# Kernel optimization log

Hardware: AMD Instinct MI355X
Metric: run time of the kernel (lower is better)

Reference implementation:

```python
import jax, jax.numpy as jnp
import numpy as np

MASK_VAL = -1e18


def _soft_nn(src, src_mask, tgt, tgt_mask):
    """score[b,i,j] = -mean_d (src[b,i,d]-tgt[b,j,d])^2, masked softmax over j,
    then soft nearest neighbor = weights @ tgt.  Uses the |a|^2+|b|^2-2ab
    expansion instead of materializing the [B,M,N,D] broadcast tensor."""
    D = src.shape[-1]
    sq_s = jnp.sum(src * src, axis=-1)                 # [B,M]
    sq_t = jnp.sum(tgt * tgt, axis=-1)                 # [B,N]
    dots = jnp.einsum('bid,bjd->bij', src, tgt)        # [B,M,N]
    dist = (sq_s[:, :, None] + sq_t[:, None, :] - 2.0 * dots) / D
    valid = (src_mask[:, :, None] > 0) & (tgt_mask[:, None, :] > 0)
    score = jnp.where(valid, -dist, MASK_VAL)
    weights = jax.nn.softmax(score, axis=-1)           # [B,M,N]
    nn = jnp.einsum('bij,bjd->bid', weights, tgt)      # [B,M,D]
    return nn, weights


def _cycle_loss(mask, lens, beta):
    """Expected index under beta vs. original index; only the diagonal of the
    original [B,M,M] distance matrix survives, so compute it directly."""
    M = mask.shape[-1]
    idx = jnp.arange(M, dtype=beta.dtype)              # [M]
    index_nn = jnp.einsum('j,bij->bi', idx, beta)      # [B,M]
    l_seq = jnp.square(index_nn - idx[None, :]) * (mask > 0)  # diag of masked dist
    return jnp.mean(jnp.sum(l_seq, axis=-1) / lens)


def setup_inputs() -> dict:
    key = jax.random.key(0)
    kce, kse, kcl, ksl = jax.random.split(key, 4)
    B, M, N, D = 32, 1024, 1024, 128
    clip_lens = jax.random.randint(kcl, (B,), M // 2, M + 1)
    sent_lens = jax.random.randint(ksl, (B,), N // 2, N + 1)
    # original code requires max(lens) == padded length (idx_orig broadcast)
    clip_lens = clip_lens.at[0].set(M)
    sent_lens = sent_lens.at[0].set(N)
    clip_mask = (jnp.arange(M)[None, :] < clip_lens[:, None]).astype(jnp.float32)
    sent_mask = (jnp.arange(N)[None, :] < sent_lens[:, None]).astype(jnp.float32)
    return {
        'clip_emb': jax.random.normal(kce, (B, M, D), dtype=jnp.float32),
        'clip_mask': clip_mask,
        'clip_lens': clip_lens.astype(jnp.float32),
        'sent_emb': jax.random.normal(kse, (B, N, D), dtype=jnp.float32),
        'sent_mask': sent_mask,
        'sent_lens': sent_lens.astype(jnp.float32),
    }


def reference(clip_emb, clip_mask, clip_lens, sent_emb, sent_mask, sent_lens):
    # clip -> sent -> clip cycle
    clip_sent_nn, _ = _soft_nn(clip_emb, clip_mask, sent_emb, sent_mask)
    _, clip_beta = _soft_nn(clip_sent_nn, clip_mask, clip_emb, clip_mask)
    clip_clip_loss = _cycle_loss(clip_mask, clip_lens, clip_beta)
    # sent -> clip -> sent cycle
    sent_clip_nn, _ = _soft_nn(sent_emb, sent_mask, clip_emb, clip_mask)
    _, sent_beta = _soft_nn(sent_clip_nn, sent_mask, sent_emb, sent_mask)
    sent_sent_loss = _cycle_loss(sent_mask, sent_lens, sent_beta)
    return (clip_clip_loss, sent_sent_loss)
```

## Files before the change

### kernel.cpp

```cpp
#include <hip/hip_runtime.h>
#include <hip/hip_bf16.h>
#include <math.h>

typedef __attribute__((ext_vector_type(16))) float f32x16;
typedef __attribute__((ext_vector_type(8))) short short8;
typedef __attribute__((ext_vector_type(4))) short short4v;
typedef __attribute__((ext_vector_type(4))) unsigned uint4v;

#define BATCH 32
#define SEQ 1024
#define DIM 128
#define NBLK 512
#define TILE_BYTES 16384
#define CDOT 0.02254211097f
#define SQE_SCALE 0.011271055485f

__device__ __forceinline__ float exp2f_fast(float x) {
  float r;
  asm("v_exp_f32 %0, %1" : "=v"(r) : "v"(x));
  return r;
}

__device__ __forceinline__ unsigned cvt_pk_bf16(float lo, float hi) {
  unsigned r;
  asm("v_cvt_pk_bf16_f32 %0, %1, %2" : "=v"(r) : "v"(lo), "v"(hi));
  return r;
}

__device__ __forceinline__ unsigned vs_off(int j, int k) {
  return ((unsigned)(k >> 4) << 11) + ((unsigned)j << 5)
       + ((((unsigned)(k & 15)) << 1) ^ ((((unsigned)j >> 2) & 1) << 4));
}

__device__ __forceinline__ short4v ds_tr16(unsigned addr) {
  short4v r;
  asm volatile("ds_read_b64_tr_b16 %0, %1" : "=v"(r) : "v"(addr));
  return r;
}

typedef __attribute__((address_space(1))) const unsigned int gu32;
typedef __attribute__((address_space(3))) unsigned int lu32;
__device__ __forceinline__ void gload_lds16(const void* g, void* l) {
  __builtin_amdgcn_global_load_lds((gu32*)g, (lu32*)l, 16, 0, 0);
}

__global__ __launch_bounds__(256)
void prepack_kernel(const float* __restrict__ clip, const float* __restrict__ sent,
                    char* __restrict__ outN, float* __restrict__ sqe_all) {
  const int bid = blockIdx.x;
  const int tid = threadIdx.x;
  const float* inp = (bid < NBLK) ? clip : sent;
  const size_t row0 = (size_t)(bid & (NBLK - 1)) * 64;
  char* ot = outN + (size_t)bid * TILE_BYTES;
  #pragma unroll
  for (int it = 0; it < 8; ++it) {
    int idx = it * 256 + tid;
    int j = idx >> 5, q = idx & 31;
    float4 v = *reinterpret_cast<const float4*>(inp + (row0 + j) * DIM + q * 4);
    uint2 pk;
    pk.x = cvt_pk_bf16(v.x, v.y);
    pk.y = cvt_pk_bf16(v.z, v.w);
    *reinterpret_cast<uint2*>(ot + vs_off(j, q * 4)) = pk;
    float s = v.x * v.x + v.y * v.y + v.z * v.z + v.w * v.w;
    #pragma unroll
    for (int off = 1; off < 32; off <<= 1) s += __shfl_xor(s, off);
    if ((tid & 31) == 0) sqe_all[bid * 64 + j] = s * SQE_SCALE;
  }
}

__global__ __launch_bounds__(256, 2)
void cycle_kernel(const char* __restrict__ embN, const float* __restrict__ sqe_all,
                  const float* __restrict__ clip_lens, const float* __restrict__ sent_lens,
                  float* __restrict__ partials)
{
  __shared__ __align__(16) char VS[2][TILE_BYTES];
  __shared__ __align__(16) float SQL[2][SEQ];
  __shared__ __align__(16) char MG[32768];
  __shared__ float RED[4][4][64];

  const int tid = threadIdx.x;
  const int x = blockIdx.x;
  const int rest = x >> 3;
  const int b    = (x & 7) + 8 * ((rest >> 2) & 3);
  const int cyc  = (rest >> 4) & 1;
  const int qh   = (rest & 3) | (((rest >> 5) & 1) << 2);

  const char* srcN = embN + (cyc ? (size_t)NBLK * TILE_BYTES : 0);
  const char* othN = embN + (cyc ? 0 : (size_t)NBLK * TILE_BYTES);
  const float* sqe_src = sqe_all + (cyc ? BATCH * SEQ : 0) + b * SEQ;
  const float* sqe_oth = sqe_all + (cyc ? 0 : BATCH * SEQ) + b * SEQ;
  const float* lens_src = cyc ? sent_lens : clip_lens;
  const float* lens_oth = cyc ? clip_lens : sent_lens;

  const int w = tid >> 6, l = tid & 63;
  const int p = w >> 1, h = w & 1;
  const int il = l & 31, hi = l >> 5, g1 = (l >> 4) & 1;

  const char* src_tiles = srcN + (size_t)(b * 16) * TILE_BYTES;
  const char* oth_tiles = othN + (size_t)(b * 16) * TILE_BYTES;

  const int nv1 = (int)(lens_oth[b] + 0.5f);
  const int nv2 = (int)(lens_src[b] + 0.5f);
  const int nt1 = (nv1 + 63) >> 6;
  const int nt2 = (nv2 + 63) >> 6;

  auto STAGE = [&](int buf, const char* gt) {
    #pragma unroll
    for (int i = 0; i < 4; ++i)
      gload_lds16(gt + i * 4096 + tid * 16, &VS[buf][i * 4096 + tid * 16]);
  };

  STAGE(0, oth_tiles);
  {
    float4 vo = reinterpret_cast<const float4*>(sqe_oth)[tid];
    float4 vq = reinterpret_cast<const float4*>(sqe_src)[tid];
    reinterpret_cast<float4*>(&SQL[0][0])[tid] = vo;
    reinterpret_cast<float4*>(&SQL[1][0])[tid] = vq;
  }

  const unsigned qk0 = (unsigned)(il * 32 + ((hi * 16) ^ (((il >> 2) & 1) << 4)));
  const int t16 = (l & 8) ? -16 : 16;

  short8 aq[2][8];
  {
    const char* qt = src_tiles + (size_t)(qh * 2 + p) * TILE_BYTES;
    #pragma unroll
    for (int s = 0; s < 2; ++s) {
      const unsigned qoff = (unsigned)((s * 32 + il) * 32
                            + ((hi * 16) ^ (((il >> 2) & 1) << 4)));
      #pragma unroll
      for (int kc = 0; kc < 8; ++kc)
        aq[s][kc] = *reinterpret_cast<const short8*>(qt + qoff + kc * 2048);
    }
  }

  f32x16 nn[2][4];
  #pragma unroll
  for (int s = 0; s < 2; ++s)
    #pragma unroll
    for (int d = 0; d < 4; ++d)
      #pragma unroll
      for (int r = 0; r < 16; ++r) nn[s][d][r] = 0.f;
  float lsum[2] = {0.f, 0.f};

  asm volatile("s_waitcnt vmcnt(0)" ::: "memory");
  __syncthreads();

  int cur = 0;
  for (int t = 0; t < nt1; ++t) {
    const int jb = t * 64;
    if (t + 1 < nt1) STAGE(cur ^ 1, oth_tiles + (size_t)(t + 1) * TILE_BYTES);
    else             STAGE(cur ^ 1, src_tiles);

    const char* vsc = &VS[cur][0];
    const unsigned vsb = (unsigned)(size_t)vsc;
    const unsigned trb0 = vsb + (unsigned)(g1 * 1920);
    const unsigned trb1 = trb0 + (unsigned)(128 + t16);
    const bool partial = (jb + h * 32 + 32) > nv1;

    f32x16 sa0, sa1;
    #pragma unroll
    for (int r = 0; r < 16; ++r) { sa0[r] = 0.f; sa1[r] = 0.f; }
    __builtin_amdgcn_s_setprio(1);
    #pragma unroll
    for (int kc = 0; kc < 8; ++kc) {
      short8 ka = *reinterpret_cast<const short8*>(vsc + qk0 + h * 1024 + kc * 2048);
      sa0 = __builtin_amdgcn_mfma_f32_32x32x16_bf16(ka, aq[0][kc], sa0, 0, 0, 0);
      sa1 = __builtin_amdgcn_mfma_f32_32x32x16_bf16(ka, aq[1][kc], sa1, 0, 0, 0);
    }
    __builtin_amdgcn_s_setprio(0);
    #pragma unroll
    for (int q = 0; q < 4; ++q) {
      float4 sq4 = *reinterpret_cast<const float4*>(&SQL[0][jb + h * 32 + q * 8 + hi * 4]);
      sa0[q*4+0] = exp2f_fast(fmaf(sa0[q*4+0], CDOT, -sq4.x));
      sa0[q*4+1] = exp2f_fast(fmaf(sa0[q*4+1], CDOT, -sq4.y));
      sa0[q*4+2] = exp2f_fast(fmaf(sa0[q*4+2], CDOT, -sq4.z));
      sa0[q*4+3] = exp2f_fast(fmaf(sa0[q*4+3], CDOT, -sq4.w));
      sa1[q*4+0] = exp2f_fast(fmaf(sa1[q*4+0], CDOT, -sq4.x));
      sa1[q*4+1] = exp2f_fast(fmaf(sa1[q*4+1], CDOT, -sq4.y));
      sa1[q*4+2] = exp2f_fast(fmaf(sa1[q*4+2], CDOT, -sq4.z));
      sa1[q*4+3] = exp2f_fast(fmaf(sa1[q*4+3], CDOT, -sq4.w));
    }
    if (partial) {
      #pragma unroll
      for (int r = 0; r < 16; ++r) {
        int j = jb + h * 32 + (r & 3) + 8 * (r >> 2) + 4 * hi;
        if (j >= nv1) { sa0[r] = 0.f; sa1[r] = 0.f; }
      }
    }
    float ls0 = 0.f, ls1 = 0.f;
    #pragma unroll
    for (int r = 0; r < 16; ++r) { ls0 += sa0[r]; ls1 += sa1[r]; }
    lsum[0] += ls0; lsum[1] += ls1;

    #pragma unroll
    for (int gm = 0; gm < 2; ++gm) {
      const int kap = h * 2 + gm;
      short4v t0[4], t1[4];
      #pragma unroll
      for (int dblk = 0; dblk < 4; ++dblk) {
        t0[dblk] = ds_tr16(trb0 + (unsigned)(dblk * 4096 + kap * 512));
        t1[dblk] = ds_tr16(trb1 + (unsigned)(dblk * 4096 + kap * 512));
      }
      unsigned a00 = cvt_pk_bf16(sa0[gm*8+0], sa0[gm*8+1]);
      unsigned a01 = cvt_pk_bf16(sa0[gm*8+2], sa0[gm*8+3]);
      unsigned a10 = cvt_pk_bf16(sa0[gm*8+4], sa0[gm*8+5]);
      unsigned a11 = cvt_pk_bf16(sa0[gm*8+6], sa0[gm*8+7]);
      asm volatile("v_permlane32_swap_b32 %0, %1" : "+v"(a00), "+v"(a10));
      asm volatile("v_permlane32_swap_b32 %0, %1" : "+v"(a01), "+v"(a11));
      uint4v pw0; pw0.x = a00; pw0.y = a01; pw0.z = a10; pw0.w = a11;
      short8 paf0 = __builtin_bit_cast(short8, pw0);
      unsigned b00 = cvt_pk_bf16(sa1[gm*8+0], sa1[gm*8+1]);
      unsigned b01 = cvt_pk_bf16(sa1[gm*8+2], sa1[gm*8+3]);
      unsigned b10 = cvt_pk_bf16(sa1[gm*8+4], sa1[gm*8+5]);
      unsigned b11 = cvt_pk_bf16(sa1[gm*8+6], sa1[gm*8+7]);
      asm volatile("v_permlane32_swap_b32 %0, %1" : "+v"(b00), "+v"(b10));
      asm volatile("v_permlane32_swap_b32 %0, %1" : "+v"(b01), "+v"(b11));
      uint4v pw1; pw1.x = b00; pw1.y = b01; pw1.z = b10; pw1.w = b11;
      short8 paf1 = __builtin_bit_cast(short8, pw1);

      asm volatile("s_waitcnt lgkmcnt(0)" ::: "memory");
      __builtin_amdgcn_sched_barrier(0);
      __builtin_amdgcn_s_setprio(1);
      #pragma unroll
      for (int dblk = 0; dblk < 4; ++dblk) {
        short8 vf = __builtin_shufflevector(t0[dblk], t1[dblk], 0, 1, 2, 3, 4, 5, 6, 7);
        nn[0][dblk] = __builtin_amdgcn_mfma_f32_32x32x16_bf16(vf, paf0, nn[0][dblk], 0, 0, 0);
        nn[1][dblk] = __builtin_amdgcn_mfma_f32_32x32x16_bf16(vf, paf1, nn[1][dblk], 0, 0, 0);
      }
      __builtin_amdgcn_s_setprio(0);
    }

    asm volatile("s_waitcnt vmcnt(0)" ::: "memory");
    __syncthreads();
    cur ^= 1;
  }

  RED[w][0][l] = lsum[0];
  RED[w][1][l] = lsum[1];
  #pragma unroll
  for (int c = 0; c < 4; ++c) {
    const int s = c >> 1, d0 = (c & 1) * 2;
    #pragma unroll
    for (int hf = 0; hf < 2; ++hf) {
      const f32x16 v = nn[s][d0 + hf];
      #pragma unroll
      for (int i = 0; i < 4; ++i) {
        float4 f4;
        f4.x = v[i*4+0]; f4.y = v[i*4+1]; f4.z = v[i*4+2]; f4.w = v[i*4+3];
        *reinterpret_cast<float4*>(MG + w * 8192 + (hf * 4 + i) * 1024 + l * 16) = f4;
      }
    }
    __syncthreads();
    #pragma unroll
    for (int hf = 0; hf < 2; ++hf) {
      #pragma unroll
      for (int i = 0; i < 4; ++i) {
        float4 f4 = *reinterpret_cast<const float4*>(
            MG + (w ^ 1) * 8192 + (hf * 4 + i) * 1024 + l * 16);
        nn[s][d0+hf][i*4+0] += f4.x;
        nn[s][d0+hf][i*4+1] += f4.y;
        nn[s][d0+hf][i*4+2] += f4.z;
        nn[s][d0+hf][i*4+3] += f4.w;
      }
    }
    __syncthreads();
  }
  lsum[0] += RED[w ^ 1][0][l];
  lsum[1] += RED[w ^ 1][1][l];

  short8 aq2[2][8];
  #pragma unroll
  for (int s = 0; s < 2; ++s) {
    lsum[s] += __shfl_xor(lsum[s], 32);
    const float inv1 = 1.f / lsum[s];
    #pragma unroll
    for (int kc = 0; kc < 8; ++kc) {
      const int dblk = kc >> 1, gm = kc & 1;
      unsigned u00 = cvt_pk_bf16(nn[s][dblk][gm*8+0] * inv1, nn[s][dblk][gm*8+1] * inv1);
      unsigned u01 = cvt_pk_bf16(nn[s][dblk][gm*8+2] * inv1, nn[s][dblk][gm*8+3] * inv1);
      unsigned u10 = cvt_pk_bf16(nn[s][dblk][gm*8+4] * inv1, nn[s][dblk][gm*8+5] * inv1);
      unsigned u11 = cvt_pk_bf16(nn[s][dblk][gm*8+6] * inv1, nn[s][dblk][gm*8+7] * inv1);
      asm volatile("v_permlane32_swap_b32 %0, %1" : "+v"(u00), "+v"(u10));
      asm volatile("v_permlane32_swap_b32 %0, %1" : "+v"(u01), "+v"(u11));
      uint4v pw; pw.x = u00; pw.y = u01; pw.z = u10; pw.w = u11;
      aq2[s][kc] = __builtin_bit_cast(short8, pw);
    }
  }

  float l2s[2] = {0.f, 0.f}, ixs[2] = {0.f, 0.f};
  for (int t = 0; t < nt2; ++t) {
    const int jb = t * 64;
    if (t + 1 < nt2) STAGE(cur ^ 1, src_tiles + (size_t)(t + 1) * TILE_BYTES);

    const char* vsc = &VS[cur][0];
    const bool partial = (jb + h * 32 + 32) > nv2;

    f32x16 sa0, sa1;
    #pragma unroll
    for (int r = 0; r < 16; ++r) { sa0[r] = 0.f; sa1[r] = 0.f; }
    __builtin_amdgcn_s_setprio(1);
    #pragma unroll
    for (int kc = 0; kc < 8; ++kc) {
      short8 ka = *reinterpret_cast<const short8*>(vsc + qk0 + h * 1024 + kc * 2048);
      sa0 = __builtin_amdgcn_mfma_f32_32x32x16_bf16(ka, aq2[0][kc], sa0, 0, 0, 0);
      sa1 = __builtin_amdgcn_mfma_f32_32x32x16_bf16(ka, aq2[1][kc], sa1, 0, 0, 0);
    }
    __builtin_amdgcn_s_setprio(0);
    #pragma unroll
    for (int q = 0; q < 4; ++q) {
      float4 sq4 = *reinterpret_cast<const float4*>(&SQL[1][jb + h * 32 + q * 8 + hi * 4]);
      sa0[q*4+0] = exp2f_fast(fmaf(sa0[q*4+0], CDOT, -sq4.x));
      sa0[q*4+1] = exp2f_fast(fmaf(sa0[q*4+1], CDOT, -sq4.y));
      sa0[q*4+2] = exp2f_fast(fmaf(sa0[q*4+2], CDOT, -sq4.z));
      sa0[q*4+3] = exp2f_fast(fmaf(sa0[q*4+3], CDOT, -sq4.w));
      sa1[q*4+0] = exp2f_fast(fmaf(sa1[q*4+0], CDOT, -sq4.x));
      sa1[q*4+1] = exp2f_fast(fmaf(sa1[q*4+1], CDOT, -sq4.y));
      sa1[q*4+2] = exp2f_fast(fmaf(sa1[q*4+2], CDOT, -sq4.z));
      sa1[q*4+3] = exp2f_fast(fmaf(sa1[q*4+3], CDOT, -sq4.w));
    }
    if (partial) {
      #pragma unroll
      for (int r = 0; r < 16; ++r) {
        int j = jb + h * 32 + (r & 3) + 8 * (r >> 2) + 4 * hi;
        if (j >= nv2) { sa0[r] = 0.f; sa1[r] = 0.f; }
      }
    }
    #pragma unroll
    for (int r = 0; r < 16; ++r) {
      float jc = (float)(jb + h * 32 + (r & 3) + 8 * (r >> 2) + 4 * hi);
      l2s[0] += sa0[r];
      l2s[1] += sa1[r];
      ixs[0] = fmaf(sa0[r], jc, ixs[0]);
      ixs[1] = fmaf(sa1[r], jc, ixs[1]);
    }

    asm volatile("s_waitcnt vmcnt(0)" ::: "memory");
    __syncthreads();
    cur ^= 1;
  }

  RED[w][0][l] = l2s[0]; RED[w][1][l] = l2s[1];
  RED[w][2][l] = ixs[0]; RED[w][3][l] = ixs[1];
  __syncthreads();
  l2s[0] += RED[w ^ 1][0][l]; l2s[1] += RED[w ^ 1][1][l];
  ixs[0] += RED[w ^ 1][2][l]; ixs[1] += RED[w ^ 1][3][l];

  float acc = 0.f;
  #pragma unroll
  for (int s = 0; s < 2; ++s) {
    l2s[s] += __shfl_xor(l2s[s], 32);
    ixs[s] += __shfl_xor(ixs[s], 32);
    int iabs = qh * 128 + p * 64 + s * 32 + il;
    float diff = ixs[s] / l2s[s] - (float)iabs;
    acc += (iabs < nv2) ? diff * diff : 0.f;
  }
  #pragma unroll
  for (int off = 1; off < 32; off <<= 1) acc += __shfl_xor(acc, off);
  if (h == 0 && l == 0)
    partials[cyc * 512 + (b * 8 + qh) * 2 + p] = acc / ((float)nv2 * (float)BATCH);
}

__global__ void reduce_kernel(const float* __restrict__ partials, float* __restrict__ out) {
  __shared__ float red[256];
  const int c = blockIdx.x;
  float s = 0.f;
  for (int i = threadIdx.x; i < 512; i += 256) s += partials[c * 512 + i];
  red[threadIdx.x] = s;
  __syncthreads();
  for (int off = 128; off > 0; off >>= 1) {
    if (threadIdx.x < off) red[threadIdx.x] += red[threadIdx.x + off];
    __syncthreads();
  }
  if (threadIdx.x == 0) out[c] = red[0];
}

extern "C" void kernel_launch(void* const* d_in, const int* in_sizes, int n_in,
                              void* d_out, int out_size, void* d_ws, size_t ws_size,
                              hipStream_t stream) {
  const float* clip_emb  = (const float*)d_in[0];
  const float* clip_lens = (const float*)d_in[2];
  const float* sent_emb  = (const float*)d_in[3];
  const float* sent_lens = (const float*)d_in[5];
  float* out = (float*)d_out;
  char* wsb = (char*)d_ws;

  char*  embN    = wsb;
  float* sqe_all = (float*)(wsb + 2 * (size_t)NBLK * TILE_BYTES);
  float* parts   = sqe_all + 2 * BATCH * SEQ;

  prepack_kernel<<<2 * NBLK, 256, 0, stream>>>(clip_emb, sent_emb, embN, sqe_all);
  cycle_kernel<<<NBLK, 256, 0, stream>>>(embN, sqe_all, clip_lens, sent_lens, parts);
  reduce_kernel<<<2, 256, 0, stream>>>(parts, out);
}
```

Measured before the change: 77.67 us.

## Stage 128-row tiles per barrier and reuse staging LDS for merge

Each pipeline stage now loads two 64-row tiles (32 KB) per buffer and processes them as two sub-tiles, halving the number of block-wide barriers and vmcnt waits in both cycle loops. The separate merge buffer is dropped; the cross-wave nn reduction reuses the idle staging buffer, so total LDS stays about the same. The s_setprio hints are removed and the transposed LDS reads are issued after the bf16 packing rather than before. In exchange, prefetch granularity is coarser, so more rows past the valid length may be loaded, and each stage has a longer unrolled body.

```diff
diff --git a/kernel.cpp b/kernel.cpp
--- a/kernel.cpp
+++ b/kernel.cpp
@@ -73,9 +73,8 @@
                   const float* __restrict__ clip_lens, const float* __restrict__ sent_lens,
                   float* __restrict__ partials)
 {
-  __shared__ __align__(16) char VS[2][TILE_BYTES];
+  __shared__ __align__(16) char VS[2][32768];
   __shared__ __align__(16) float SQL[2][SEQ];
-  __shared__ __align__(16) char MG[32768];
   __shared__ float RED[4][4][64];
 
   const int tid = threadIdx.x;
@@ -101,12 +100,12 @@
 
   const int nv1 = (int)(lens_oth[b] + 0.5f);
   const int nv2 = (int)(lens_src[b] + 0.5f);
-  const int nt1 = (nv1 + 63) >> 6;
-  const int nt2 = (nv2 + 63) >> 6;
+  const int nt1_2 = (nv1 + 127) >> 7;
+  const int nt2_2 = (nv2 + 127) >> 7;
 
   auto STAGE = [&](int buf, const char* gt) {
     #pragma unroll
-    for (int i = 0; i < 4; ++i)
+    for (int i = 0; i < 8; ++i)
       gload_lds16(gt + i * 4096 + tid * 16, &VS[buf][i * 4096 + tid * 16]);
   };
 
@@ -147,88 +146,89 @@
   __syncthreads();
 
   int cur = 0;
-  for (int t = 0; t < nt1; ++t) {
-    const int jb = t * 64;
-    if (t + 1 < nt1) STAGE(cur ^ 1, oth_tiles + (size_t)(t + 1) * TILE_BYTES);
-    else             STAGE(cur ^ 1, src_tiles);
-
-    const char* vsc = &VS[cur][0];
-    const unsigned vsb = (unsigned)(size_t)vsc;
-    const unsigned trb0 = vsb + (unsigned)(g1 * 1920);
-    const unsigned trb1 = trb0 + (unsigned)(128 + t16);
-    const bool partial = (jb + h * 32 + 32) > nv1;
-
-    f32x16 sa0, sa1;
-    #pragma unroll
-    for (int r = 0; r < 16; ++r) { sa0[r] = 0.f; sa1[r] = 0.f; }
-    __builtin_amdgcn_s_setprio(1);
-    #pragma unroll
-    for (int kc = 0; kc < 8; ++kc) {
-      short8 ka = *reinterpret_cast<const short8*>(vsc + qk0 + h * 1024 + kc * 2048);
-      sa0 = __builtin_amdgcn_mfma_f32_32x32x16_bf16(ka, aq[0][kc], sa0, 0, 0, 0);
-      sa1 = __builtin_amdgcn_mfma_f32_32x32x16_bf16(ka, aq[1][kc], sa1, 0, 0, 0);
-    }
-    __builtin_amdgcn_s_setprio(0);
-    #pragma unroll
-    for (int q = 0; q < 4; ++q) {
-      float4 sq4 = *reinterpret_cast<const float4*>(&SQL[0][jb + h * 32 + q * 8 + hi * 4]);
-      sa0[q*4+0] = exp2f_fast(fmaf(sa0[q*4+0], CDOT, -sq4.x));
-      sa0[q*4+1] = exp2f_fast(fmaf(sa0[q*4+1], CDOT, -sq4.y));
-      sa0[q*4+2] = exp2f_fast(fmaf(sa0[q*4+2], CDOT, -sq4.z));
-      sa0[q*4+3] = exp2f_fast(fmaf(sa0[q*4+3], CDOT, -sq4.w));
-      sa1[q*4+0] = exp2f_fast(fmaf(sa1[q*4+0], CDOT, -sq4.x));
-      sa1[q*4+1] = exp2f_fast(fmaf(sa1[q*4+1], CDOT, -sq4.y));
-      sa1[q*4+2] = exp2f_fast(fmaf(sa1[q*4+2], CDOT, -sq4.z));
-      sa1[q*4+3] = exp2f_fast(fmaf(sa1[q*4+3], CDOT, -sq4.w));
-    }
-    if (partial) {
-      #pragma unroll
-      for (int r = 0; r < 16; ++r) {
-        int j = jb + h * 32 + (r & 3) + 8 * (r >> 2) + 4 * hi;
-        if (j >= nv1) { sa0[r] = 0.f; sa1[r] = 0.f; }
+  for (int t = 0; t < nt1_2; ++t) {
+    if (t + 1 < nt1_2) STAGE(cur ^ 1, oth_tiles + (size_t)(t + 1) * 32768);
+    else               STAGE(cur ^ 1, src_tiles);
+
+    #pragma unroll
+    for (int sub = 0; sub < 2; ++sub) {
+      const int jb = t * 128 + sub * 64;
+      if (jb < nv1) {
+        const char* vsc = &VS[cur][0] + sub * 16384;
+        const unsigned vsb = (unsigned)(size_t)vsc;
+        const unsigned trb0 = vsb + (unsigned)(g1 * 1920);
+        const unsigned trb1 = trb0 + (unsigned)(128 + t16);
+        const bool partial = (jb + h * 32 + 32) > nv1;
+
+        f32x16 sa0, sa1;
+        #pragma unroll
+        for (int r = 0; r < 16; ++r) { sa0[r] = 0.f; sa1[r] = 0.f; }
+        #pragma unroll
+        for (int kc = 0; kc < 8; ++kc) {
+          short8 ka = *reinterpret_cast<const short8*>(vsc + qk0 + h * 1024 + kc * 2048);
+          sa0 = __builtin_amdgcn_mfma_f32_32x32x16_bf16(ka, aq[0][kc], sa0, 0, 0, 0);
+          sa1 = __builtin_amdgcn_mfma_f32_32x32x16_bf16(ka, aq[1][kc], sa1, 0, 0, 0);
+        }
+        #pragma unroll
+        for (int q = 0; q < 4; ++q) {
+          float4 sq4 = *reinterpret_cast<const float4*>(&SQL[0][jb + h * 32 + q * 8 + hi * 4]);
+          sa0[q*4+0] = exp2f_fast(fmaf(sa0[q*4+0], CDOT, -sq4.x));
+          sa0[q*4+1] = exp2f_fast(fmaf(sa0[q*4+1], CDOT, -sq4.y));
+          sa0[q*4+2] = exp2f_fast(fmaf(sa0[q*4+2], CDOT, -sq4.z));
+          sa0[q*4+3] = exp2f_fast(fmaf(sa0[q*4+3], CDOT, -sq4.w));
+          sa1[q*4+0] = exp2f_fast(fmaf(sa1[q*4+0], CDOT, -sq4.x));
+          sa1[q*4+1] = exp2f_fast(fmaf(sa1[q*4+1], CDOT, -sq4.y));
+          sa1[q*4+2] = exp2f_fast(fmaf(sa1[q*4+2], CDOT, -sq4.z));
+          sa1[q*4+3] = exp2f_fast(fmaf(sa1[q*4+3], CDOT, -sq4.w));
+        }
+        if (partial) {
+          #pragma unroll
+          for (int r = 0; r < 16; ++r) {
+            int j = jb + h * 32 + (r & 3) + 8 * (r >> 2) + 4 * hi;
+            if (j >= nv1) { sa0[r] = 0.f; sa1[r] = 0.f; }
+          }
+        }
+        float ls0 = 0.f, ls1 = 0.f;
+        #pragma unroll
+        for (int r = 0; r < 16; ++r) { ls0 += sa0[r]; ls1 += sa1[r]; }
+        lsum[0] += ls0; lsum[1] += ls1;
+
+        #pragma unroll
+        for (int gm = 0; gm < 2; ++gm) {
+          const int kap = h * 2 + gm;
+          unsigned a00 = cvt_pk_bf16(sa0[gm*8+0], sa0[gm*8+1]);
+          unsigned a01 = cvt_pk_bf16(sa0[gm*8+2], sa0[gm*8+3]);
+          unsigned a10 = cvt_pk_bf16(sa0[gm*8+4], sa0[gm*8+5]);
+          unsigned a11 = cvt_pk_bf16(sa0[gm*8+6], sa0[gm*8+7]);
+          asm volatile("v_permlane32_swap_b32 %0, %1" : "+v"(a00), "+v"(a10));
+          asm volatile("v_permlane32_swap_b32 %0, %1" : "+v"(a01), "+v"(a11));
+          uint4v pw0; pw0.x = a00; pw0.y = a01; pw0.z = a10; pw0.w = a11;
+          short8 paf0 = __builtin_bit_cast(short8, pw0);
+          unsigned b00 = cvt_pk_bf16(sa1[gm*8+0], sa1[gm*8+1]);
+          unsigned b01 = cvt_pk_bf16(sa1[gm*8+2], sa1[gm*8+3]);
+          unsigned b10 = cvt_pk_bf16(sa1[gm*8+4], sa1[gm*8+5]);
+          unsigned b11 = cvt_pk_bf16(sa1[gm*8+6], sa1[gm*8+7]);
+          asm volatile("v_permlane32_swap_b32 %0, %1" : "+v"(b00), "+v"(b10));
+          asm volatile("v_permlane32_swap_b32 %0, %1" : "+v"(b01), "+v"(b11));
+          uint4v pw1; pw1.x = b00; pw1.y = b01; pw1.z = b10; pw1.w = b11;
+          short8 paf1 = __builtin_bit_cast(short8, pw1);
+
+          short4v t0[4], t1[4];
+          #pragma unroll
+          for (int dblk = 0; dblk < 4; ++dblk) {
+            t0[dblk] = ds_tr16(trb0 + (unsigned)(dblk * 4096 + kap * 512));
+            t1[dblk] = ds_tr16(trb1 + (unsigned)(dblk * 4096 + kap * 512));
+          }
+          asm volatile("s_waitcnt lgkmcnt(0)" ::: "memory");
+          __builtin_amdgcn_sched_barrier(0);
+          #pragma unroll
+          for (int dblk = 0; dblk < 4; ++dblk) {
+            short8 vf = __builtin_shufflevector(t0[dblk], t1[dblk], 0, 1, 2, 3, 4, 5, 6, 7);
+            nn[0][dblk] = __builtin_amdgcn_mfma_f32_32x32x16_bf16(vf, paf0, nn[0][dblk], 0, 0, 0);
+            nn[1][dblk] = __builtin_amdgcn_mfma_f32_32x32x16_bf16(vf, paf1, nn[1][dblk], 0, 0, 0);
+          }
+        }
       }
-    }
-    float ls0 = 0.f, ls1 = 0.f;
-    #pragma unroll
-    for (int r = 0; r < 16; ++r) { ls0 += sa0[r]; ls1 += sa1[r]; }
-    lsum[0] += ls0; lsum[1] += ls1;
-
-    #pragma unroll
-    for (int gm = 0; gm < 2; ++gm) {
-      const int kap = h * 2 + gm;
-      short4v t0[4], t1[4];
-      #pragma unroll
-      for (int dblk = 0; dblk < 4; ++dblk) {
-        t0[dblk] = ds_tr16(trb0 + (unsigned)(dblk * 4096 + kap * 512));
-        t1[dblk] = ds_tr16(trb1 + (unsigned)(dblk * 4096 + kap * 512));
-      }
-      unsigned a00 = cvt_pk_bf16(sa0[gm*8+0], sa0[gm*8+1]);
-      unsigned a01 = cvt_pk_bf16(sa0[gm*8+2], sa0[gm*8+3]);
-      unsigned a10 = cvt_pk_bf16(sa0[gm*8+4], sa0[gm*8+5]);
-      unsigned a11 = cvt_pk_bf16(sa0[gm*8+6], sa0[gm*8+7]);
-      asm volatile("v_permlane32_swap_b32 %0, %1" : "+v"(a00), "+v"(a10));
-      asm volatile("v_permlane32_swap_b32 %0, %1" : "+v"(a01), "+v"(a11));
-      uint4v pw0; pw0.x = a00; pw0.y = a01; pw0.z = a10; pw0.w = a11;
-      short8 paf0 = __builtin_bit_cast(short8, pw0);
-      unsigned b00 = cvt_pk_bf16(sa1[gm*8+0], sa1[gm*8+1]);
-      unsigned b01 = cvt_pk_bf16(sa1[gm*8+2], sa1[gm*8+3]);
-      unsigned b10 = cvt_pk_bf16(sa1[gm*8+4], sa1[gm*8+5]);
-      unsigned b11 = cvt_pk_bf16(sa1[gm*8+6], sa1[gm*8+7]);
-      asm volatile("v_permlane32_swap_b32 %0, %1" : "+v"(b00), "+v"(b10));
-      asm volatile("v_permlane32_swap_b32 %0, %1" : "+v"(b01), "+v"(b11));
-      uint4v pw1; pw1.x = b00; pw1.y = b01; pw1.z = b10; pw1.w = b11;
-      short8 paf1 = __builtin_bit_cast(short8, pw1);
-
-      asm volatile("s_waitcnt lgkmcnt(0)" ::: "memory");
-      __builtin_amdgcn_sched_barrier(0);
-      __builtin_amdgcn_s_setprio(1);
-      #pragma unroll
-      for (int dblk = 0; dblk < 4; ++dblk) {
-        short8 vf = __builtin_shufflevector(t0[dblk], t1[dblk], 0, 1, 2, 3, 4, 5, 6, 7);
-        nn[0][dblk] = __builtin_amdgcn_mfma_f32_32x32x16_bf16(vf, paf0, nn[0][dblk], 0, 0, 0);
-        nn[1][dblk] = __builtin_amdgcn_mfma_f32_32x32x16_bf16(vf, paf1, nn[1][dblk], 0, 0, 0);
-      }
-      __builtin_amdgcn_s_setprio(0);
     }
 
     asm volatile("s_waitcnt vmcnt(0)" ::: "memory");
@@ -238,6 +238,7 @@
 
   RED[w][0][l] = lsum[0];
   RED[w][1][l] = lsum[1];
+  char* const mg = &VS[cur ^ 1][0];
   #pragma unroll
   for (int c = 0; c < 4; ++c) {
     const int s = c >> 1, d0 = (c & 1) * 2;
@@ -248,7 +249,7 @@
       for (int i = 0; i < 4; ++i) {
         float4 f4;
         f4.x = v[i*4+0]; f4.y = v[i*4+1]; f4.z = v[i*4+2]; f4.w = v[i*4+3];
-        *reinterpret_cast<float4*>(MG + w * 8192 + (hf * 4 + i) * 1024 + l * 16) = f4;
+        *reinterpret_cast<float4*>(mg + w * 8192 + (hf * 4 + i) * 1024 + l * 16) = f4;
       }
     }
     __syncthreads();
@@ -257,7 +258,7 @@
       #pragma unroll
       for (int i = 0; i < 4; ++i) {
         float4 f4 = *reinterpret_cast<const float4*>(
-            MG + (w ^ 1) * 8192 + (hf * 4 + i) * 1024 + l * 16);
+            mg + (w ^ 1) * 8192 + (hf * 4 + i) * 1024 + l * 16);
         nn[s][d0+hf][i*4+0] += f4.x;
         nn[s][d0+hf][i*4+1] += f4.y;
         nn[s][d0+hf][i*4+2] += f4.z;
@@ -289,50 +290,53 @@
   }
 
   float l2s[2] = {0.f, 0.f}, ixs[2] = {0.f, 0.f};
-  for (int t = 0; t < nt2; ++t) {
-    const int jb = t * 64;
-    if (t + 1 < nt2) STAGE(cur ^ 1, src_tiles + (size_t)(t + 1) * TILE_BYTES);
-
-    const char* vsc = &VS[cur][0];
-    const bool partial = (jb + h * 32 + 32) > nv2;
-
-    f32x16 sa0, sa1;
-    #pragma unroll
-    for (int r = 0; r < 16; ++r) { sa0[r] = 0.f; sa1[r] = 0.f; }
-    __builtin_amdgcn_s_setprio(1);
-    #pragma unroll
-    for (int kc = 0; kc < 8; ++kc) {
-      short8 ka = *reinterpret_cast<const short8*>(vsc + qk0 + h * 1024 + kc * 2048);
-      sa0 = __builtin_amdgcn_mfma_f32_32x32x16_bf16(ka, aq2[0][kc], sa0, 0, 0, 0);
-      sa1 = __builtin_amdgcn_mfma_f32_32x32x16_bf16(ka, aq2[1][kc], sa1, 0, 0, 0);
-    }
-    __builtin_amdgcn_s_setprio(0);
-    #pragma unroll
-    for (int q = 0; q < 4; ++q) {
-      float4 sq4 = *reinterpret_cast<const float4*>(&SQL[1][jb + h * 32 + q * 8 + hi * 4]);
-      sa0[q*4+0] = exp2f_fast(fmaf(sa0[q*4+0], CDOT, -sq4.x));
-      sa0[q*4+1] = exp2f_fast(fmaf(sa0[q*4+1], CDOT, -sq4.y));
-      sa0[q*4+2] = exp2f_fast(fmaf(sa0[q*4+2], CDOT, -sq4.z));
-      sa0[q*4+3] = exp2f_fast(fmaf(sa0[q*4+3], CDOT, -sq4.w));
-      sa1[q*4+0] = exp2f_fast(fmaf(sa1[q*4+0], CDOT, -sq4.x));
-      sa1[q*4+1] = exp2f_fast(fmaf(sa1[q*4+1], CDOT, -sq4.y));
-      sa1[q*4+2] = exp2f_fast(fmaf(sa1[q*4+2], CDOT, -sq4.z));
-      sa1[q*4+3] = exp2f_fast(fmaf(sa1[q*4+3], CDOT, -sq4.w));
-    }
-    if (partial) {
-      #pragma unroll
-      for (int r = 0; r < 16; ++r) {
-        int j = jb + h * 32 + (r & 3) + 8 * (r >> 2) + 4 * hi;
-        if (j >= nv2) { sa0[r] = 0.f; sa1[r] = 0.f; }
+  for (int t = 0; t < nt2_2; ++t) {
+    if (t + 1 < nt2_2) STAGE(cur ^ 1, src_tiles + (size_t)(t + 1) * 32768);
+
+    #pragma unroll
+    for (int sub = 0; sub < 2; ++sub) {
+      const int jb = t * 128 + sub * 64;
+      if (jb < nv2) {
+        const char* vsc = &VS[cur][0] + sub * 16384;
+        const bool partial = (jb + h * 32 + 32) > nv2;
+
+        f32x16 sa0, sa1;
+        #pragma unroll
+        for (int r = 0; r < 16; ++r) { sa0[r] = 0.f; sa1[r] = 0.f; }
+        #pragma unroll
+        for (int kc = 0; kc < 8; ++kc) {
+          short8 ka = *reinterpret_cast<const short8*>(vsc + qk0 + h * 1024 + kc * 2048);
+          sa0 = __builtin_amdgcn_mfma_f32_32x32x16_bf16(ka, aq2[0][kc], sa0, 0, 0, 0);
+          sa1 = __builtin_amdgcn_mfma_f32_32x32x16_bf16(ka, aq2[1][kc], sa1, 0, 0, 0);
+        }
+        #pragma unroll
+        for (int q = 0; q < 4; ++q) {
+          float4 sq4 = *reinterpret_cast<const float4*>(&SQL[1][jb + h * 32 + q * 8 + hi * 4]);
+          sa0[q*4+0] = exp2f_fast(fmaf(sa0[q*4+0], CDOT, -sq4.x));
+          sa0[q*4+1] = exp2f_fast(fmaf(sa0[q*4+1], CDOT, -sq4.y));
+          sa0[q*4+2] = exp2f_fast(fmaf(sa0[q*4+2], CDOT, -sq4.z));
+          sa0[q*4+3] = exp2f_fast(fmaf(sa0[q*4+3], CDOT, -sq4.w));
+          sa1[q*4+0] = exp2f_fast(fmaf(sa1[q*4+0], CDOT, -sq4.x));
+          sa1[q*4+1] = exp2f_fast(fmaf(sa1[q*4+1], CDOT, -sq4.y));
+          sa1[q*4+2] = exp2f_fast(fmaf(sa1[q*4+2], CDOT, -sq4.z));
+          sa1[q*4+3] = exp2f_fast(fmaf(sa1[q*4+3], CDOT, -sq4.w));
+        }
+        if (partial) {
+          #pragma unroll
+          for (int r = 0; r < 16; ++r) {
+            int j = jb + h * 32 + (r & 3) + 8 * (r >> 2) + 4 * hi;
+            if (j >= nv2) { sa0[r] = 0.f; sa1[r] = 0.f; }
+          }
+        }
+        #pragma unroll
+        for (int r = 0; r < 16; ++r) {
+          float jc = (float)(jb + h * 32 + (r & 3) + 8 * (r >> 2) + 4 * hi);
+          l2s[0] += sa0[r];
+          l2s[1] += sa1[r];
+          ixs[0] = fmaf(sa0[r], jc, ixs[0]);
+          ixs[1] = fmaf(sa1[r], jc, ixs[1]);
+        }
       }
-    }
-    #pragma unroll
-    for (int r = 0; r < 16; ++r) {
-      float jc = (float)(jb + h * 32 + (r & 3) + 8 * (r >> 2) + 4 * hi);
-      l2s[0] += sa0[r];
-      l2s[1] += sa1[r];
-      ixs[0] = fmaf(sa0[r], jc, ixs[0]);
-      ixs[1] = fmaf(sa1[r], jc, ixs[1]);
     }
 
     asm volatile("s_waitcnt vmcnt(0)" ::: "memory");
```

Result: no change. 77.26 us (-0.5%).
